# Kernel tuning notes

Hardware: AMD Instinct MI355X
Metric: run time of the kernel (lower is better)

Reference implementation:

```python
import jax, jax.numpy as jnp
import numpy as np

N_NODES = 100000
N_EDGES = 800000
IN_FEATS = 128
N_HIDDEN = 128
N_CLASSES = 64


def setup_inputs() -> dict:
    key = jax.random.key(0)
    k = jax.random.split(key, 6)
    x = jax.random.normal(k[0], (N_NODES, IN_FEATS), dtype=jnp.float32)
    src = jax.random.randint(k[1], (N_EDGES,), 0, N_NODES, dtype=jnp.int32)
    dst = jax.random.randint(k[2], (N_EDGES,), 0, N_NODES, dtype=jnp.int32)
    W_neigh = jax.random.normal(k[3], (IN_FEATS, N_HIDDEN), dtype=jnp.float32) * (1.0 / np.sqrt(IN_FEATS))
    b_neigh = jnp.zeros((N_HIDDEN,), dtype=jnp.float32)
    W_out = jax.random.normal(k[4], (N_HIDDEN, N_CLASSES), dtype=jnp.float32) * (1.0 / np.sqrt(N_HIDDEN))
    b_out = jnp.zeros((N_CLASSES,), dtype=jnp.float32)
    return {"x": x, "src": src, "dst": dst, "W_neigh": W_neigh, "b_neigh": b_neigh,
            "W_out": W_out, "b_out": b_out}


def reference(x, src, dst, W_neigh, b_neigh, W_out, b_out):
    # DGL SAGEConv with 'gcn' aggregator:
    #   h_neigh[v] = (sum_{u->v} x[u] + x[v]) / (in_deg(v) + 1)
    #   h = h_neigh @ W_neigh + b_neigh
    deg = jax.ops.segment_sum(jnp.ones_like(dst, dtype=x.dtype), dst, num_segments=N_NODES)
    agg = jax.ops.segment_sum(x[src], dst, num_segments=N_NODES)  # [N, F] irregular gather+scatter
    h_neigh = (agg + x) / (deg + 1.0)[:, None]
    h = h_neigh @ W_neigh + b_neigh
    emb = jax.nn.relu(h)
    # dropout is identity in eval/reference mode
    out = emb @ W_out + b_out
    return (out, emb)
```

## Files before the change

kernel.cpp:

```cpp
#include <hip/hip_runtime.h>
#include <hip/hip_bf16.h>

#define N_NODES 100000
#define N_EDGES 800000
#define F 128
#define C_OUT 64
#define CAP 48

typedef __bf16 bf16x8 __attribute__((ext_vector_type(8)));
typedef __bf16 bf16x4 __attribute__((ext_vector_type(4)));
typedef __bf16 bf16x2 __attribute__((ext_vector_type(2)));
typedef float f32x4 __attribute__((ext_vector_type(4)));

__global__ __launch_bounds__(256) void prep(const float* __restrict__ x,
                                            const int* __restrict__ src,
                                            const int* __restrict__ dst,
                                            float* __restrict__ emb,
                                            int* __restrict__ cnt,
                                            const float* __restrict__ Wn,
                                            const float* __restrict__ Wo,
                                            __bf16* __restrict__ Wn_s,
                                            __bf16* __restrict__ Wo_s,
                                            __bf16* __restrict__ xb) {
    const int t = blockIdx.x * 256 + threadIdx.x;

#pragma unroll
    for (int k = 0; k < 4; k++) {
        const int i = k * 800000 + t;
        const float4 v = ((const float4*)x)[i];
        bf16x4 b;
        b.x = (__bf16)v.x; b.y = (__bf16)v.y; b.z = (__bf16)v.z; b.w = (__bf16)v.w;
        *(bf16x4*)(xb + (size_t)i * 4) = b;
    }

    const int d = dst[t];
    const int slot = atomicAdd(cnt + d, 1);
    if (slot < CAP) ((int*)(emb + (size_t)d * F))[slot] = src[t];

    if (t < 3072) {
        const float* W;
        __bf16* Ws;
        int g, ncols;
        if (t < 2048) { W = Wn; Ws = Wn_s; g = t;        ncols = 128; }
        else          { W = Wo; Ws = Wo_s; g = t - 2048; ncols = 64;  }
        const int l = g & 63;
        const int kb = (g >> 6) & 3;
        const int nb = g >> 8;
        const int q = l >> 4, m = l & 15;
        const int n = nb * 16 + m;
        __bf16 v[8];
#pragma unroll
        for (int j = 0; j < 8; j++) {
            const int k = kb * 32 + q * 8 + j;
            v[j] = (__bf16)W[(size_t)k * ncols + n];
        }
        *(bf16x8*)(Ws + (size_t)g * 8) = *(bf16x8*)v;
    }
}

#define ACC4(bk, j, acc)                                                      \
    {                                                                         \
        const int4 s4 = *(const int4*)((bk) + (j));                           \
        const bf16x2 v0 = *(const bf16x2*)(xb + (size_t)s4.x * F + 2 * lane); \
        const bf16x2 v1 = *(const bf16x2*)(xb + (size_t)s4.y * F + 2 * lane); \
        const bf16x2 v2 = *(const bf16x2*)(xb + (size_t)s4.z * F + 2 * lane); \
        const bf16x2 v3 = *(const bf16x2*)(xb + (size_t)s4.w * F + 2 * lane); \
        acc.x += (float)v0.x + (float)v1.x + (float)v2.x + (float)v3.x;       \
        acc.y += (float)v0.y + (float)v1.y + (float)v2.y + (float)v3.y;       \
    }

#define ACC1(bk, j, acc)                                                       \
    {                                                                          \
        const int s = (bk)[j];                                                 \
        const bf16x2 v = *(const bf16x2*)(xb + (size_t)s * F + 2 * lane);      \
        acc.x += (float)v.x;                                                   \
        acc.y += (float)v.y;                                                   \
    }

__global__ __launch_bounds__(256, 8) void sage1(const __bf16* __restrict__ xb,
                                                const int* __restrict__ cnt,
                                                const __bf16* __restrict__ Wn_s,
                                                const float* __restrict__ bn,
                                                float* emb) {
    __shared__ __align__(16) __bf16 Hs[4][16][136];
    const int w = threadIdx.x >> 6;
    const int lane = threadIdx.x & 63;
    const int node0 = (blockIdx.x * 4 + w) * 16;
    if (node0 >= N_NODES) return;
    const int q = lane >> 4, m = lane & 15;
    __bf16(*H)[136] = Hs[w];

    for (int i = 0; i < 16; i += 2) {
        const int nodeA = node0 + i, nodeB = nodeA + 1;
        const int degA = cnt[nodeA], degB = cnt[nodeB];
        const int nA = degA < CAP ? degA : CAP;
        const int nB = degB < CAP ? degB : CAP;
        const bf16x2 sA = *(const bf16x2*)(xb + (size_t)nodeA * F + 2 * lane);
        const bf16x2 sB = *(const bf16x2*)(xb + (size_t)nodeB * F + 2 * lane);
        float2 accA = make_float2((float)sA.x, (float)sA.y);
        float2 accB = make_float2((float)sB.x, (float)sB.y);
        const int* bkA = (const int*)(emb + (size_t)nodeA * F);
        const int* bkB = (const int*)(emb + (size_t)nodeB * F);
        int ja = 0, jb = 0;
        while ((ja + 4 <= nA) && (jb + 4 <= nB)) {
            ACC4(bkA, ja, accA);
            ACC4(bkB, jb, accB);
            ja += 4; jb += 4;
        }
        while (ja + 4 <= nA) { ACC4(bkA, ja, accA); ja += 4; }
        while (jb + 4 <= nB) { ACC4(bkB, jb, accB); jb += 4; }
        while ((ja < nA) && (jb < nB)) { ACC1(bkA, ja, accA); ACC1(bkB, jb, accB); ja++; jb++; }
        while (ja < nA) { ACC1(bkA, ja, accA); ja++; }
        while (jb < nB) { ACC1(bkB, jb, accB); jb++; }

        const float invA = 1.0f / (float)(degA + 1);
        const float invB = 1.0f / (float)(degB + 1);
        bf16x2 hA, hB;
        hA.x = (__bf16)(accA.x * invA); hA.y = (__bf16)(accA.y * invA);
        hB.x = (__bf16)(accB.x * invB); hB.y = (__bf16)(accB.y * invB);
        *(bf16x2*)&H[i][2 * lane] = hA;
        *(bf16x2*)&H[i + 1][2 * lane] = hB;
    }

    bf16x8 a[4];
#pragma unroll
    for (int kb = 0; kb < 4; kb++)
        a[kb] = *(const bf16x8*)&H[m][kb * 32 + q * 8];
    asm volatile("s_waitcnt lgkmcnt(0)" ::: "memory");

    float* Ef = (float*)&H[0][0];
    const int srow = lane >> 2;
    const int sc4 = (lane & 3) * 4;
#pragma unroll
    for (int half = 0; half < 2; half++) {
#pragma unroll
        for (int nb2 = 0; nb2 < 4; nb2++) {
            const int nb = half * 4 + nb2;
            f32x4 c = {0.f, 0.f, 0.f, 0.f};
#pragma unroll
            for (int kb = 0; kb < 4; kb++) {
                const bf16x8 b = *(const bf16x8*)(Wn_s + ((size_t)(nb * 4 + kb) * 64 + lane) * 8);
                c = __builtin_amdgcn_mfma_f32_16x16x32_bf16(a[kb], b, c, 0, 0, 0);
            }
            const float bias = bn[nb * 16 + m];
#pragma unroll
            for (int r = 0; r < 4; r++)
                Ef[(q * 4 + r) * 68 + nb2 * 16 + m] = fmaxf(c[r] + bias, 0.f);
        }
        asm volatile("s_waitcnt lgkmcnt(0)" ::: "memory");
#pragma unroll
        for (int it = 0; it < 4; it++) {
            const f32x4 v = *(const f32x4*)&Ef[srow * 68 + it * 16 + sc4];
            *(f32x4*)&emb[(size_t)(node0 + srow) * F + half * 64 + it * 16 + sc4] = v;
        }
        if (half == 0) asm volatile("s_waitcnt lgkmcnt(0)" ::: "memory");
    }
}

__global__ __launch_bounds__(256, 6) void sage2(const float* __restrict__ emb,
                                                const __bf16* __restrict__ Wo_s,
                                                const float* __restrict__ bo,
                                                float* __restrict__ out) {
    const int w = threadIdx.x >> 6;
    const int lane = threadIdx.x & 63;
    const int node0 = (blockIdx.x * 4 + w) * 16;
    if (node0 >= N_NODES) return;
    const int q = lane >> 4, m = lane & 15;

    bf16x8 a[4];
#pragma unroll
    for (int kb = 0; kb < 4; kb++) {
        const float* p = emb + (size_t)(node0 + m) * F + kb * 32 + q * 8;
        const float4 f0 = *(const float4*)(p);
        const float4 f1 = *(const float4*)(p + 4);
        bf16x8 v;
        v[0] = (__bf16)f0.x; v[1] = (__bf16)f0.y; v[2] = (__bf16)f0.z; v[3] = (__bf16)f0.w;
        v[4] = (__bf16)f1.x; v[5] = (__bf16)f1.y; v[6] = (__bf16)f1.z; v[7] = (__bf16)f1.w;
        a[kb] = v;
    }

#pragma unroll
    for (int nb = 0; nb < 4; nb++) {
        f32x4 c = {0.f, 0.f, 0.f, 0.f};
#pragma unroll
        for (int kb = 0; kb < 4; kb++) {
            const bf16x8 b = *(const bf16x8*)(Wo_s + ((size_t)(nb * 4 + kb) * 64 + lane) * 8);
            c = __builtin_amdgcn_mfma_f32_16x16x32_bf16(a[kb], b, c, 0, 0, 0);
        }
        const int col = nb * 16 + m;
        const float bias = bo[col];
#pragma unroll
        for (int r = 0; r < 4; r++) {
            const int node = node0 + q * 4 + r;
            out[(size_t)node * C_OUT + col] = c[r] + bias;
        }
    }
}

extern "C" void kernel_launch(void* const* d_in, const int* in_sizes, int n_in,
                              void* d_out, int out_size, void* d_ws, size_t ws_size,
                              hipStream_t stream) {
    const float* x  = (const float*)d_in[0];
    const int* src  = (const int*)d_in[1];
    const int* dst  = (const int*)d_in[2];
    const float* Wn = (const float*)d_in[3];
    const float* bn = (const float*)d_in[4];
    const float* Wo = (const float*)d_in[5];
    const float* bo = (const float*)d_in[6];

    float* out = (float*)d_out;
    float* emb = out + (size_t)N_NODES * C_OUT;
    __bf16* xb = (__bf16*)d_out;

    int* cnt = (int*)d_ws;
    __bf16* Wn_s = (__bf16*)((char*)d_ws + 400000);
    __bf16* Wo_s = Wn_s + 128 * 128;

    hipMemsetAsync(cnt, 0, N_NODES * sizeof(int), stream);

    prep<<<3125, 256, 0, stream>>>(x, src, dst, emb, cnt, Wn, Wo, Wn_s, Wo_s, xb);

    sage1<<<(N_NODES + 63) / 64, 256, 0, stream>>>(xb, cnt, Wn_s, bn, emb);

    sage2<<<(N_NODES + 63) / 64, 256, 0, stream>>>(emb, Wo_s, bo, out);
}
```

Before: 219.7 us.

## Fuse both SAGE GEMM stages into one kernel with padded 4-node gather

Adds a fused kernel that aggregates neighbours, computes emb with the first MFMA GEMM, and immediately feeds the ReLU output from LDS into the second GEMM to write out. This removes the separate sage2 pass, which re-read emb from global memory. The bf16 copy of x moves into workspace so it no longer aliases out, and a zeroed dummy row is appended. Neighbour lists are padded to multiples of 4 with that dummy index, so four nodes are gathered together without scalar tails. The original three-kernel path remains as a fallback when the workspace is too small, and the fused kernel's lower occupancy bound (6 vs 8) may reduce latency hiding in the gather phase.

```diff
diff --git a/kernel.cpp b/kernel.cpp
--- a/kernel.cpp
+++ b/kernel.cpp
@@ -6,6 +6,7 @@
 #define F 128
 #define C_OUT 64
 #define CAP 48
+#define DUMMY N_NODES
 
 typedef __bf16 bf16x8 __attribute__((ext_vector_type(8)));
 typedef __bf16 bf16x4 __attribute__((ext_vector_type(4)));
@@ -21,7 +22,8 @@
                                             const float* __restrict__ Wo,
                                             __bf16* __restrict__ Wn_s,
                                             __bf16* __restrict__ Wo_s,
-                                            __bf16* __restrict__ xb) {
+                                            __bf16* __restrict__ xb,
+                                            int zero_dummy) {
     const int t = blockIdx.x * 256 + threadIdx.x;
 
 #pragma unroll
@@ -31,6 +33,11 @@
         bf16x4 b;
         b.x = (__bf16)v.x; b.y = (__bf16)v.y; b.z = (__bf16)v.z; b.w = (__bf16)v.w;
         *(bf16x4*)(xb + (size_t)i * 4) = b;
+    }
+
+    if (zero_dummy && t < 32) {
+        int2 z = make_int2(0, 0);
+        ((int2*)(xb + (size_t)N_NODES * F))[t] = z;
     }
 
     const int d = dst[t];
@@ -77,11 +84,143 @@
         acc.y += (float)v.y;                                                   \
     }
 
-__global__ __launch_bounds__(256, 8) void sage1(const __bf16* __restrict__ xb,
-                                                const int* __restrict__ cnt,
-                                                const __bf16* __restrict__ Wn_s,
-                                                const float* __restrict__ bn,
-                                                float* emb) {
+__global__ __launch_bounds__(256, 6) void sage_fused(const __bf16* __restrict__ xb,
+                                                     const int* __restrict__ cnt,
+                                                     const __bf16* __restrict__ Wn_s,
+                                                     const __bf16* __restrict__ Wo_s,
+                                                     const float* __restrict__ bn,
+                                                     const float* __restrict__ bo,
+                                                     float* __restrict__ out,
+                                                     float* emb) {
+    __shared__ __align__(16) __bf16 Hs[4][16][136];
+    const int w = threadIdx.x >> 6;
+    const int lane = threadIdx.x & 63;
+    const int node0 = (blockIdx.x * 4 + w) * 16;
+    if (node0 >= N_NODES) return;
+    const int q = lane >> 4, m = lane & 15;
+    __bf16(*H)[136] = Hs[w];
+
+    for (int i = 0; i < 16; i += 4) {
+        const int na = node0 + i;
+        const int4 dg = *(const int4*)(cnt + na);
+        const int n0 = dg.x < CAP ? dg.x : CAP, n1 = dg.y < CAP ? dg.y : CAP;
+        const int n2 = dg.z < CAP ? dg.z : CAP, n3 = dg.w < CAP ? dg.w : CAP;
+        const int p0 = (n0 + 3) & ~3, p1 = (n1 + 3) & ~3;
+        const int p2 = (n2 + 3) & ~3, p3 = (n3 + 3) & ~3;
+        const int* bk0 = (const int*)(emb + (size_t)(na + 0) * F);
+        const int* bk1 = (const int*)(emb + (size_t)(na + 1) * F);
+        const int* bk2 = (const int*)(emb + (size_t)(na + 2) * F);
+        const int* bk3 = (const int*)(emb + (size_t)(na + 3) * F);
+        const bf16x2 s0 = *(const bf16x2*)(xb + (size_t)(na + 0) * F + 2 * lane);
+        const bf16x2 s1 = *(const bf16x2*)(xb + (size_t)(na + 1) * F + 2 * lane);
+        const bf16x2 s2 = *(const bf16x2*)(xb + (size_t)(na + 2) * F + 2 * lane);
+        const bf16x2 s3 = *(const bf16x2*)(xb + (size_t)(na + 3) * F + 2 * lane);
+        if (lane < 4) {
+            const int nn = lane == 0 ? n0 : lane == 1 ? n1 : lane == 2 ? n2 : n3;
+            const int pp = lane == 0 ? p0 : lane == 1 ? p1 : lane == 2 ? p2 : p3;
+            int* bw = (int*)(lane == 0 ? bk0 : lane == 1 ? bk1 : lane == 2 ? bk2 : bk3);
+            for (int s = nn; s < pp; s++) bw[s] = DUMMY;
+        }
+        asm volatile("s_waitcnt vmcnt(0)" ::: "memory");
+
+        float2 a0 = make_float2((float)s0.x, (float)s0.y);
+        float2 a1 = make_float2((float)s1.x, (float)s1.y);
+        float2 a2 = make_float2((float)s2.x, (float)s2.y);
+        float2 a3 = make_float2((float)s3.x, (float)s3.y);
+        const int jmax = max(max(p0, p1), max(p2, p3));
+        for (int j = 0; j < jmax; j += 4) {
+            if (j < p0) ACC4(bk0, j, a0);
+            if (j < p1) ACC4(bk1, j, a1);
+            if (j < p2) ACC4(bk2, j, a2);
+            if (j < p3) ACC4(bk3, j, a3);
+        }
+        const float i0 = 1.0f / (float)(dg.x + 1), i1 = 1.0f / (float)(dg.y + 1);
+        const float i2 = 1.0f / (float)(dg.z + 1), i3 = 1.0f / (float)(dg.w + 1);
+        bf16x2 h0, h1, h2, h3;
+        h0.x = (__bf16)(a0.x * i0); h0.y = (__bf16)(a0.y * i0);
+        h1.x = (__bf16)(a1.x * i1); h1.y = (__bf16)(a1.y * i1);
+        h2.x = (__bf16)(a2.x * i2); h2.y = (__bf16)(a2.y * i2);
+        h3.x = (__bf16)(a3.x * i3); h3.y = (__bf16)(a3.y * i3);
+        *(bf16x2*)&H[i + 0][2 * lane] = h0;
+        *(bf16x2*)&H[i + 1][2 * lane] = h1;
+        *(bf16x2*)&H[i + 2][2 * lane] = h2;
+        *(bf16x2*)&H[i + 3][2 * lane] = h3;
+    }
+
+    bf16x8 afr[4];
+#pragma unroll
+    for (int kb = 0; kb < 4; kb++)
+        afr[kb] = *(const bf16x8*)&H[m][kb * 32 + q * 8];
+    asm volatile("s_waitcnt lgkmcnt(0)" ::: "memory");
+
+    float* Ef = (float*)&H[0][0];
+    const int srow = lane >> 2;
+    const int sc4 = (lane & 3) * 4;
+    f32x4 o[4];
+#pragma unroll
+    for (int nb = 0; nb < 4; nb++) o[nb] = (f32x4){0.f, 0.f, 0.f, 0.f};
+
+#pragma unroll
+    for (int half = 0; half < 2; half++) {
+#pragma unroll
+        for (int nb2 = 0; nb2 < 4; nb2++) {
+            const int nb = half * 4 + nb2;
+            f32x4 c = {0.f, 0.f, 0.f, 0.f};
+#pragma unroll
+            for (int kb = 0; kb < 4; kb++) {
+                const bf16x8 b = *(const bf16x8*)(Wn_s + ((size_t)(nb * 4 + kb) * 64 + lane) * 8);
+                c = __builtin_amdgcn_mfma_f32_16x16x32_bf16(afr[kb], b, c, 0, 0, 0);
+            }
+            const float bias = bn[nb * 16 + m];
+#pragma unroll
+            for (int r = 0; r < 4; r++)
+                Ef[(q * 4 + r) * 68 + nb2 * 16 + m] = fmaxf(c[r] + bias, 0.f);
+        }
+        asm volatile("s_waitcnt lgkmcnt(0)" ::: "memory");
+#pragma unroll
+        for (int it = 0; it < 4; it++) {
+            const f32x4 v = *(const f32x4*)&Ef[srow * 68 + it * 16 + sc4];
+            *(f32x4*)&emb[(size_t)(node0 + srow) * F + half * 64 + it * 16 + sc4] = v;
+        }
+#pragma unroll
+        for (int t2 = 0; t2 < 2; t2++) {
+            const int kb = half * 2 + t2;
+            const f32x4 f0 = *(const f32x4*)&Ef[m * 68 + t2 * 32 + q * 8];
+            const f32x4 f1 = *(const f32x4*)&Ef[m * 68 + t2 * 32 + q * 8 + 4];
+            bf16x8 a2f;
+            a2f[0] = (__bf16)f0[0]; a2f[1] = (__bf16)f0[1];
+            a2f[2] = (__bf16)f0[2]; a2f[3] = (__bf16)f0[3];
+            a2f[4] = (__bf16)f1[0]; a2f[5] = (__bf16)f1[1];
+            a2f[6] = (__bf16)f1[2]; a2f[7] = (__bf16)f1[3];
+#pragma unroll
+            for (int nb = 0; nb < 4; nb++) {
+                const bf16x8 b = *(const bf16x8*)(Wo_s + ((size_t)(nb * 4 + kb) * 64 + lane) * 8);
+                o[nb] = __builtin_amdgcn_mfma_f32_16x16x32_bf16(a2f, b, o[nb], 0, 0, 0);
+            }
+        }
+        asm volatile("s_waitcnt lgkmcnt(0)" ::: "memory");
+    }
+
+#pragma unroll
+    for (int nb = 0; nb < 4; nb++) {
+        const float bias = bo[nb * 16 + m];
+#pragma unroll
+        for (int r = 0; r < 4; r++)
+            Ef[(q * 4 + r) * 68 + nb * 16 + m] = o[nb][r] + bias;
+    }
+    asm volatile("s_waitcnt lgkmcnt(0)" ::: "memory");
+#pragma unroll
+    for (int it = 0; it < 4; it++) {
+        const f32x4 v = *(const f32x4*)&Ef[srow * 68 + it * 16 + sc4];
+        *(f32x4*)&out[(size_t)(node0 + srow) * C_OUT + it * 16 + sc4] = v;
+    }
+}
+
+__global__ __launch_bounds__(256, 8) void sage1_fb(const __bf16* __restrict__ xb,
+                                                   const int* __restrict__ cnt,
+                                                   const __bf16* __restrict__ Wn_s,
+                                                   const float* __restrict__ bn,
+                                                   float* emb) {
     __shared__ __align__(16) __bf16 Hs[4][16][136];
     const int w = threadIdx.x >> 6;
     const int lane = threadIdx.x & 63;
@@ -112,7 +251,6 @@
         while ((ja < nA) && (jb < nB)) { ACC1(bkA, ja, accA); ACC1(bkB, jb, accB); ja++; jb++; }
         while (ja < nA) { ACC1(bkA, ja, accA); ja++; }
         while (jb < nB) { ACC1(bkB, jb, accB); jb++; }
-
         const float invA = 1.0f / (float)(degA + 1);
         const float invB = 1.0f / (float)(degB + 1);
         bf16x2 hA, hB;
@@ -157,10 +295,10 @@
     }
 }
 
-__global__ __launch_bounds__(256, 6) void sage2(const float* __restrict__ emb,
-                                                const __bf16* __restrict__ Wo_s,
-                                                const float* __restrict__ bo,
-                                                float* __restrict__ out) {
+__global__ __launch_bounds__(256, 6) void sage2_fb(const float* __restrict__ emb,
+                                                   const __bf16* __restrict__ Wo_s,
+                                                   const float* __restrict__ bo,
+                                                   float* __restrict__ out) {
     const int w = threadIdx.x >> 6;
     const int lane = threadIdx.x & 63;
     const int node0 = (blockIdx.x * 4 + w) * 16;
@@ -178,7 +316,6 @@
         v[4] = (__bf16)f1.x; v[5] = (__bf16)f1.y; v[6] = (__bf16)f1.z; v[7] = (__bf16)f1.w;
         a[kb] = v;
     }
-
 #pragma unroll
     for (int nb = 0; nb < 4; nb++) {
         f32x4 c = {0.f, 0.f, 0.f, 0.f};
@@ -210,17 +347,27 @@
 
     float* out = (float*)d_out;
     float* emb = out + (size_t)N_NODES * C_OUT;
-    __bf16* xb = (__bf16*)d_out;
 
     int* cnt = (int*)d_ws;
     __bf16* Wn_s = (__bf16*)((char*)d_ws + 400000);
     __bf16* Wo_s = Wn_s + 128 * 128;
+    __bf16* xb_ws = (__bf16*)((char*)d_ws + 449152);
+
+    const size_t WS_NEEDED = 449152 + (size_t)(N_NODES + 1) * F * 2;
+    const bool fused = ws_size >= WS_NEEDED;
 
     hipMemsetAsync(cnt, 0, N_NODES * sizeof(int), stream);
 
-    prep<<<3125, 256, 0, stream>>>(x, src, dst, emb, cnt, Wn, Wo, Wn_s, Wo_s, xb);
-
-    sage1<<<(N_NODES + 63) / 64, 256, 0, stream>>>(xb, cnt, Wn_s, bn, emb);
-
-    sage2<<<(N_NODES + 63) / 64, 256, 0, stream>>>(emb, Wo_s, bo, out);
-}
+    if (fused) {
+        prep<<<3125, 256, 0, stream>>>(x, src, dst, emb, cnt, Wn, Wo, Wn_s, Wo_s,
+                                       xb_ws, 1);
+        sage_fused<<<(N_NODES + 63) / 64, 256, 0, stream>>>(xb_ws, cnt, Wn_s, Wo_s,
+                                                            bn, bo, out, emb);
+    } else {
+        __bf16* xb = (__bf16*)d_out;
+        prep<<<3125, 256, 0, stream>>>(x, src, dst, emb, cnt, Wn, Wo, Wn_s, Wo_s,
+                                       xb, 0);
+        sage1_fb<<<(N_NODES + 63) / 64, 256, 0, stream>>>(xb, cnt, Wn_s, bn, emb);
+        sage2_fb<<<(N_NODES + 63) / 64, 256, 0, stream>>>(emb, Wo_s, bo, out);
+    }
+}
```

Result: faster. 215.2 us (-2.1%).
